# Optimization experiments

Hardware: AMD Instinct MI355X
Metric: run time of the kernel (lower is better)

## Reference

```python
import jax, jax.numpy as jnp
import numpy as np

H = 256        # hidden_size
V = 8192       # output_size / vocab
S = 4096       # encoder source length


def _lin(x, w, b):
    # torch nn.Linear: x @ W^T + b, W shape [out, in]
    return x @ w.T + b


def setup_inputs() -> dict:
    key = jax.random.key(0)
    ks = jax.random.split(key, 32)
    f32 = jnp.float32

    def w(i, shape, scale=0.02):
        return (jax.random.normal(ks[i], shape) * scale).astype(f32)

    inp = {
        "input_tok": jax.random.randint(ks[0], (1,), 0, V),
        "hidden": jax.random.normal(ks[1], (1, H), dtype=f32),
        "encoder_outputs": jax.random.normal(ks[2], (S, 2 * H), dtype=f32),
        "emb": w(3, (V, V), 0.02),
        "Uz_w": w(4, (H, V)), "Uz_b": jnp.zeros((H,), f32),
        "Wz_w": w(5, (H, H)), "Wz_b": jnp.zeros((H,), f32),
        "Cz_w": w(6, (H, 2 * H)), "Cz_b": jnp.zeros((H,), f32),
        "Ur_w": w(7, (H, V)), "Ur_b": jnp.zeros((H,), f32),
        "Wr_w": w(8, (H, H)), "Wr_b": jnp.zeros((H,), f32),
        "Cr_w": w(9, (H, 2 * H)), "Cr_b": jnp.zeros((H,), f32),
        "Uh_w": w(10, (H, V)), "Uh_b": jnp.zeros((H,), f32),
        "Wh_w": w(11, (H, H)), "Wh_b": jnp.zeros((H,), f32),
        "Ch_w": w(12, (H, 2 * H)), "Ch_b": jnp.zeros((H,), f32),
        "Ua_w": w(13, (H, 2 * H)), "Ua_b": jnp.zeros((H,), f32),
        "Wa_w": w(14, (H, H)), "Wa_b": jnp.zeros((H,), f32),
        "Va_w": w(15, (1, H)), "Va_b": jnp.zeros((1,), f32),
        "V_w": w(16, (V, H)), "V_b": jnp.zeros((V,), f32),
    }
    return inp


def reference(input_tok, hidden, encoder_outputs, emb,
              Uz_w, Uz_b, Wz_w, Wz_b, Cz_w, Cz_b,
              Ur_w, Ur_b, Wr_w, Wr_b, Cr_w, Cr_b,
              Uh_w, Uh_b, Wh_w, Wh_b, Ch_w, Ch_b,
              Ua_w, Ua_b, Wa_w, Wa_b, Va_w, Va_b,
              V_w, V_b):
    y = emb[input_tok[0]].reshape(1, V)                                   # [1, V]
    # Bahdanau additive attention over encoder states (softmax over dim 0)
    e = jnp.tanh(_lin(hidden, Wa_w, Wa_b) + _lin(encoder_outputs, Ua_w, Ua_b))  # [S, H]
    Eij = _lin(e, Va_w, Va_b)                                             # [S, 1]
    aij = jax.nn.softmax(Eij, axis=0)                                     # [S, 1]
    Ci = jnp.sum(aij * encoder_outputs, axis=0).reshape(1, 2 * H)         # [1, 2H]
    # GRU gates
    z = jax.nn.sigmoid(_lin(y, Uz_w, Uz_b) + _lin(hidden, Wz_w, Wz_b) + _lin(Ci, Cz_w, Cz_b))
    r = jax.nn.sigmoid(_lin(y, Ur_w, Ur_b) + _lin(hidden, Wr_w, Wr_b) + _lin(Ci, Cr_w, Cr_b))
    c = jnp.tanh(_lin(y, Uh_w, Uh_b) + _lin(r * hidden, Wh_w, Wh_b) + _lin(Ci, Ch_w, Ch_b))
    hidden_new = (1.0 - z) * c + z * hidden                               # [1, H]
    out = jax.nn.log_softmax(_lin(hidden_new, V_w, V_b), axis=1)          # [1, V]
    return (out, hidden_new, aij)
```

## Files before the change

kernel.cpp:

```cpp
#include <hip/hip_runtime.h>
#include <hip/hip_bf16.h>

typedef unsigned int u32;

#define HD 256
#define VD 8192
#define SD 4096
#define H2 512

#define WS_WAH   0
#define WS_STATS 320
#define WS_CI    384
#define WS_G     896
#define WS_AZR   1664
#define WS_HN    2432
#define WS_EIJ   2688

__device__ __forceinline__ float dot4(float4 a, float4 b, float acc) {
    acc = fmaf(a.x, b.x, acc); acc = fmaf(a.y, b.y, acc);
    acc = fmaf(a.z, b.z, acc); return fmaf(a.w, b.w, acc);
}
__device__ __forceinline__ float wred64(float v) {
    #pragma unroll
    for (int o = 32; o; o >>= 1) v += __shfl_xor(v, o);
    return v;
}

__global__ __launch_bounds__(256) void ka_gates(const int* __restrict__ tok,
        const float* __restrict__ emb,
        const float* __restrict__ Uz_w, const float* __restrict__ Uz_b,
        const float* __restrict__ Wz_w, const float* __restrict__ Wz_b,
        const float* __restrict__ Ur_w, const float* __restrict__ Ur_b,
        const float* __restrict__ Wr_w, const float* __restrict__ Wr_b,
        const float* __restrict__ Uh_w, const float* __restrict__ Uh_b,
        const float* __restrict__ Wa_w, const float* __restrict__ Wa_b,
        const float* __restrict__ hidden,
        float* __restrict__ G, float* __restrict__ wa_h) {
    int t = threadIdx.x, lane = t & 63, wv = t >> 6;
    if (blockIdx.x == 192) {
        __shared__ __align__(16) float hs[HD];
        hs[t] = hidden[t];
        __syncthreads();
        float acc = 0.f;
        const float4* row = (const float4*)(Wa_w + (size_t)t * HD);
        #pragma unroll 4
        for (int k = 0; k < HD / 4; ++k)
            acc = dot4(row[k], *(const float4*)&hs[k * 4], acc);
        wa_h[t] = acc + Wa_b[t];
        return;
    }
    int wg = blockIdx.x * 4 + wv;
    int g = wg >> 8, i = wg & 255;
    const float* U = (g == 0 ? Uz_w : (g == 1 ? Ur_w : Uh_w)) + (size_t)i * VD;
    const float* y = emb + (size_t)tok[0] * VD;
    float acc = 0.f;
    for (int c = 0; c < VD; c += 512) {
        int k = c + lane * 8;
        acc = dot4(*(const float4*)(U + k),     *(const float4*)(y + k),     acc);
        acc = dot4(*(const float4*)(U + k + 4), *(const float4*)(y + k + 4), acc);
    }
    if (g < 2) {
        const float* W = (g == 0 ? Wz_w : Wr_w) + (size_t)i * HD;
        int k = lane * 4;
        acc = dot4(*(const float4*)(W + k), *(const float4*)(hidden + k), acc);
    }
    acc = wred64(acc);
    if (lane == 0) {
        float b;
        if (g == 0)      b = Uz_b[i] + Wz_b[i];
        else if (g == 1) b = Ur_b[i] + Wr_b[i];
        else             b = Uh_b[i];
        G[wg] = acc + b;
    }
}

__global__ __launch_bounds__(256) void k1_scores(const float* __restrict__ enc,
        const float* __restrict__ Ua_w, const float* __restrict__ Ua_b,
        const float* __restrict__ Va_w, const float* __restrict__ Va_b,
        const float* __restrict__ wa_h, float* __restrict__ Eij) {
    __shared__ __align__(16) float encs[16 * H2];
    int t = threadIdx.x;
    int lane = t & 63, sg = t >> 6;
    int h0 = lane * 4;
    long s0 = (long)blockIdx.x * 16;

    for (int i = t * 4; i < 16 * H2; i += 1024)
        *(float4*)&encs[i] = *(const float4*)(enc + s0 * H2 + i);
    __syncthreads();

    float acc[4][4];
    #pragma unroll
    for (int a = 0; a < 4; ++a)
        #pragma unroll
        for (int b = 0; b < 4; ++b) acc[a][b] = 0.f;

    const float* r0 = Ua_w + (size_t)(h0 + 0) * H2;
    const float* r1 = Ua_w + (size_t)(h0 + 1) * H2;
    const float* r2 = Ua_w + (size_t)(h0 + 2) * H2;
    const float* r3 = Ua_w + (size_t)(h0 + 3) * H2;
    for (int kc = 0; kc < H2; kc += 4) {
        float4 a0 = *(const float4*)(r0 + kc);
        float4 a1 = *(const float4*)(r1 + kc);
        float4 a2 = *(const float4*)(r2 + kc);
        float4 a3 = *(const float4*)(r3 + kc);
        #pragma unroll
        for (int ss = 0; ss < 4; ++ss) {
            float4 ev = *(const float4*)&encs[(sg * 4 + ss) * H2 + kc];
            acc[ss][0] = dot4(a0, ev, acc[ss][0]);
            acc[ss][1] = dot4(a1, ev, acc[ss][1]);
            acc[ss][2] = dot4(a2, ev, acc[ss][2]);
            acc[ss][3] = dot4(a3, ev, acc[ss][3]);
        }
    }

    float bias[4], va[4];
    #pragma unroll
    for (int j = 0; j < 4; ++j) {
        bias[j] = wa_h[h0 + j] + Ua_b[h0 + j];
        va[j]   = Va_w[h0 + j];
    }
    float vb = Va_b[0];
    #pragma unroll
    for (int ss = 0; ss < 4; ++ss) {
        float v = 0.f;
        #pragma unroll
        for (int j = 0; j < 4; ++j)
            v += va[j] * tanhf(acc[ss][j] + bias[j]);
        v = wred64(v);
        if (lane == 0) Eij[s0 + sg * 4 + ss] = v + vb;
    }
}

__global__ __launch_bounds__(256) void k2_stats(const float* __restrict__ Eij,
                                                float* __restrict__ stats,
                                                float* __restrict__ Ci) {
    __shared__ float sh[4];
    int t = threadIdx.x, lane = t & 63, wv = t >> 6;
    float m = -1e30f;
    for (int i = t; i < SD; i += 256) m = fmaxf(m, Eij[i]);
    #pragma unroll
    for (int o = 32; o; o >>= 1) m = fmaxf(m, __shfl_xor(m, o));
    if (lane == 0) sh[wv] = m;
    __syncthreads();
    m = fmaxf(fmaxf(sh[0], sh[1]), fmaxf(sh[2], sh[3]));
    __syncthreads();
    float s = 0.f;
    for (int i = t; i < SD; i += 256) s += __expf(Eij[i] - m);
    s = wred64(s);
    if (lane == 0) sh[wv] = s;
    __syncthreads();
    s = sh[0] + sh[1] + sh[2] + sh[3];
    if (t == 0) { stats[0] = m; stats[1] = 1.f / s; }
    for (int i = t; i < H2; i += 256) Ci[i] = 0.f;
}

__global__ __launch_bounds__(256) void k3_ci(const float* __restrict__ Eij,
                                             const float* __restrict__ stats,
                                             const float* __restrict__ enc,
                                             float* __restrict__ out,
                                             float* __restrict__ Ci) {
    __shared__ float a[64];
    int t = threadIdx.x;
    long s0 = (long)blockIdx.x * 64;
    if (t < 64) {
        float v = __expf(Eij[s0 + t] - stats[0]) * stats[1];
        a[t] = v;
        out[8448 + s0 + t] = v;
    }
    __syncthreads();
    float acc0 = 0.f, acc1 = 0.f;
    for (int s = 0; s < 64; ++s) {
        float av = a[s];
        const float* r = enc + (s0 + s) * H2;
        acc0 = fmaf(av, r[t], acc0);
        acc1 = fmaf(av, r[t + 256], acc1);
    }
    atomicAdd(Ci + t, acc0);
    atomicAdd(Ci + t + 256, acc1);
}

__global__ __launch_bounds__(256) void k5a_cdots(const float* __restrict__ G,
        const float* __restrict__ Ci,
        const float* __restrict__ Cz_w, const float* __restrict__ Cz_b,
        const float* __restrict__ Cr_w, const float* __restrict__ Cr_b,
        const float* __restrict__ Ch_w, const float* __restrict__ Ch_b,
        const float* __restrict__ Wh_b,
        float* __restrict__ AZR) {
    int t = threadIdx.x, lane = t & 63, wv = t >> 6;
    int wg = blockIdx.x * 4 + wv;
    int g = wg >> 8, i = wg & 255;
    const float* C = (g == 0 ? Cz_w : (g == 1 ? Cr_w : Ch_w)) + (size_t)i * H2;
    int k = lane * 8;
    float acc = dot4(*(const float4*)(C + k),     *(const float4*)(Ci + k),     0.f);
    acc = dot4(*(const float4*)(C + k + 4), *(const float4*)(Ci + k + 4), acc);
    acc = wred64(acc);
    if (lane == 0) {
        float b;
        if (g == 0)      b = Cz_b[i];
        else if (g == 1) b = Cr_b[i];
        else             b = Wh_b[i] + Ch_b[i];
        AZR[wg] = G[wg] + acc + b;
    }
}

__global__ __launch_bounds__(256) void k5c_hnew(const float* __restrict__ AZR,
        const float* __restrict__ Wh_w, const float* __restrict__ hidden,
        float* __restrict__ hn_f, float* __restrict__ out) {
    int t = threadIdx.x, lane = t & 63, wv = t >> 6;
    int i = blockIdx.x * 4 + wv;
    int k = lane * 4;
    float4 ar4 = *(const float4*)(AZR + 256 + k);
    float4 h4  = *(const float4*)(hidden + k);
    float4 rh;
    rh.x = h4.x / (1.f + __expf(-ar4.x));
    rh.y = h4.y / (1.f + __expf(-ar4.y));
    rh.z = h4.z / (1.f + __expf(-ar4.z));
    rh.w = h4.w / (1.f + __expf(-ar4.w));
    float acc = dot4(*(const float4*)(Wh_w + (size_t)i * HD + k), rh, 0.f);
    acc = wred64(acc);
    if (lane == 0) {
        float c = tanhf(AZR[512 + i] + acc);
        float z = 1.f / (1.f + __expf(-AZR[i]));
        float hnv = (1.f - z) * c + z * hidden[i];
        hn_f[i] = hnv;
        out[8192 + i] = hnv;
    }
}

__global__ __launch_bounds__(256) void k6_logits(const float* __restrict__ Vw,
        const float* __restrict__ Vb, const float* __restrict__ hn,
        float* __restrict__ out) {
    int t = threadIdx.x, lane = t & 63, wv = t >> 6;
    float4 h4 = *(const float4*)(hn + lane * 4);
    long r0 = ((long)blockIdx.x * 4 + wv) * 16;
    for (int rr = 0; rr < 16; ++rr) {
        long j = r0 + rr;
        float acc = dot4(*(const float4*)(Vw + j * HD + lane * 4), h4, 0.f);
        acc = wred64(acc);
        if (lane == 0) out[j] = acc + Vb[j];
    }
}

__global__ __launch_bounds__(256) void k7_lsm(float* __restrict__ out) {
    __shared__ float sh[4];
    int t = threadIdx.x, lane = t & 63, wv = t >> 6;
    float m = -1e30f;
    for (int i = t; i < VD; i += 256) m = fmaxf(m, out[i]);
    #pragma unroll
    for (int o = 32; o; o >>= 1) m = fmaxf(m, __shfl_xor(m, o));
    if (lane == 0) sh[wv] = m;
    __syncthreads();
    m = fmaxf(fmaxf(sh[0], sh[1]), fmaxf(sh[2], sh[3]));
    __syncthreads();
    float s = 0.f;
    for (int i = t; i < VD; i += 256) s += __expf(out[i] - m);
    s = wred64(s);
    if (lane == 0) sh[wv] = s;
    __syncthreads();
    s = sh[0] + sh[1] + sh[2] + sh[3];
    float lse = m + __logf(s);
    for (int i = t; i < VD; i += 256) out[i] = out[i] - lse;
}

extern "C" void kernel_launch(void* const* d_in, const int* in_sizes, int n_in,
                              void* d_out, int out_size, void* d_ws, size_t ws_size,
                              hipStream_t stream) {
    const int*   tok    = (const int*)d_in[0];
    const float* hidden = (const float*)d_in[1];
    const float* enc    = (const float*)d_in[2];
    const float* emb    = (const float*)d_in[3];
    const float* Uz_w = (const float*)d_in[4],  *Uz_b = (const float*)d_in[5];
    const float* Wz_w = (const float*)d_in[6],  *Wz_b = (const float*)d_in[7];
    const float* Cz_w = (const float*)d_in[8],  *Cz_b = (const float*)d_in[9];
    const float* Ur_w = (const float*)d_in[10], *Ur_b = (const float*)d_in[11];
    const float* Wr_w = (const float*)d_in[12], *Wr_b = (const float*)d_in[13];
    const float* Cr_w = (const float*)d_in[14], *Cr_b = (const float*)d_in[15];
    const float* Uh_w = (const float*)d_in[16], *Uh_b = (const float*)d_in[17];
    const float* Wh_w = (const float*)d_in[18], *Wh_b = (const float*)d_in[19];
    const float* Ch_w = (const float*)d_in[20], *Ch_b = (const float*)d_in[21];
    const float* Ua_w = (const float*)d_in[22], *Ua_b = (const float*)d_in[23];
    const float* Wa_w = (const float*)d_in[24], *Wa_b = (const float*)d_in[25];
    const float* Va_w = (const float*)d_in[26], *Va_b = (const float*)d_in[27];
    const float* V_w  = (const float*)d_in[28], *V_b  = (const float*)d_in[29];

    float* ws    = (float*)d_ws;
    float* wa_h  = ws + WS_WAH;
    float* stats = ws + WS_STATS;
    float* Ci    = ws + WS_CI;
    float* G     = ws + WS_G;
    float* AZR   = ws + WS_AZR;
    float* hn_f  = ws + WS_HN;
    float* Eij   = ws + WS_EIJ;
    float* out   = (float*)d_out;

    ka_gates<<<193, 256, 0, stream>>>(tok, emb, Uz_w, Uz_b, Wz_w, Wz_b,
                                      Ur_w, Ur_b, Wr_w, Wr_b, Uh_w, Uh_b,
                                      Wa_w, Wa_b, hidden, G, wa_h);
    k1_scores<<<256, 256, 0, stream>>>(enc, Ua_w, Ua_b, Va_w, Va_b, wa_h, Eij);
    k2_stats<<<1, 256, 0, stream>>>(Eij, stats, Ci);
    k3_ci<<<64, 256, 0, stream>>>(Eij, stats, enc, out, Ci);
    k5a_cdots<<<192, 256, 0, stream>>>(G, Ci, Cz_w, Cz_b, Cr_w, Cr_b,
                                       Ch_w, Ch_b, Wh_b, AZR);
    k5c_hnew<<<64, 256, 0, stream>>>(AZR, Wh_w, hidden, hn_f, out);
    k6_logits<<<128, 256, 0, stream>>>(V_w, V_b, hn_f, out);
    k7_lsm<<<1, 256, 0, stream>>>(out);
}
```

Baseline: 494.7 us.

## Fuse attention and gate kernels to cut launch count from eight to five

Merges the gate GEMV and the attention score kernel into one launch. Each score block recomputes Wa·hidden redundantly, so it no longer waits on a separate producer kernel. The softmax stats are folded into the Ci kernel, with each block recomputing max and sum, and the C-dots are merged with the h_new computation, where each block recomputes the r gate. The logits kernel also emits per-block maxima so the log-softmax skips a max pass. The aim is to remove kernel launch and serialization overhead, at the cost of redundant work per block.

Result: no change. 498.4 us (+0.8%).

```diff
diff --git a/kernel.cpp b/kernel.cpp
--- a/kernel.cpp
+++ b/kernel.cpp
@@ -1,5 +1,4 @@
 #include <hip/hip_runtime.h>
-#include <hip/hip_bf16.h>
 
 typedef unsigned int u32;
 
@@ -8,11 +7,9 @@
 #define SD 4096
 #define H2 512
 
-#define WS_WAH   0
-#define WS_STATS 320
 #define WS_CI    384
 #define WS_G     896
-#define WS_AZR   1664
+#define WS_PMAX  1664
 #define WS_HN    2432
 #define WS_EIJ   2688
 
@@ -26,7 +23,7 @@
     return v;
 }
 
-__global__ __launch_bounds__(256) void ka_gates(const int* __restrict__ tok,
+__global__ __launch_bounds__(256) void ka_front(const int* __restrict__ tok,
         const float* __restrict__ emb,
         const float* __restrict__ Uz_w, const float* __restrict__ Uz_b,
         const float* __restrict__ Wz_w, const float* __restrict__ Wz_b,
@@ -34,58 +31,61 @@
         const float* __restrict__ Wr_w, const float* __restrict__ Wr_b,
         const float* __restrict__ Uh_w, const float* __restrict__ Uh_b,
         const float* __restrict__ Wa_w, const float* __restrict__ Wa_b,
-        const float* __restrict__ hidden,
-        float* __restrict__ G, float* __restrict__ wa_h) {
-    int t = threadIdx.x, lane = t & 63, wv = t >> 6;
-    if (blockIdx.x == 192) {
-        __shared__ __align__(16) float hs[HD];
-        hs[t] = hidden[t];
-        __syncthreads();
+        const float* __restrict__ Ua_w, const float* __restrict__ Ua_b,
+        const float* __restrict__ Va_w, const float* __restrict__ Va_b,
+        const float* __restrict__ enc, const float* __restrict__ hidden,
+        float* __restrict__ G, float* __restrict__ Eij, float* __restrict__ Ci) {
+    int t = threadIdx.x, lane = t & 63, wv = t >> 6;
+
+    if (blockIdx.x >= 256) {
+        int bb = blockIdx.x - 256;
+        if (bb == 0) { Ci[t] = 0.f; Ci[t + 256] = 0.f; }
+        int wg = bb * 4 + wv;
+        int g = wg >> 8, i = wg & 255;
+        const float* U = (g == 0 ? Uz_w : (g == 1 ? Ur_w : Uh_w)) + (size_t)i * VD;
+        const float* y = emb + (size_t)tok[0] * VD;
         float acc = 0.f;
-        const float4* row = (const float4*)(Wa_w + (size_t)t * HD);
+        for (int c = 0; c < VD; c += 512) {
+            int k = c + lane * 8;
+            acc = dot4(*(const float4*)(U + k),     *(const float4*)(y + k),     acc);
+            acc = dot4(*(const float4*)(U + k + 4), *(const float4*)(y + k + 4), acc);
+        }
+        if (g < 2) {
+            const float* W = (g == 0 ? Wz_w : Wr_w) + (size_t)i * HD;
+            int k = lane * 4;
+            acc = dot4(*(const float4*)(W + k), *(const float4*)(hidden + k), acc);
+        }
+        acc = wred64(acc);
+        if (lane == 0) {
+            float b;
+            if (g == 0)      b = Uz_b[i] + Wz_b[i];
+            else if (g == 1) b = Ur_b[i] + Wr_b[i];
+            else             b = Uh_b[i];
+            G[wg] = acc + b;
+        }
+        return;
+    }
+
+    __shared__ __align__(16) float encs[16 * H2];
+    __shared__ __align__(16) float hs[HD];
+    __shared__ float wah[HD];
+    int sg = wv;
+    int h0 = lane * 4;
+    long s0 = (long)blockIdx.x * 16;
+
+    for (int i = t * 4; i < 16 * H2; i += 1024)
+        *(float4*)&encs[i] = *(const float4*)(enc + s0 * H2 + i);
+    hs[t] = hidden[t];
+    __syncthreads();
+
+    {
+        float wacc = 0.f;
+        const float4* wrow = (const float4*)(Wa_w + (size_t)t * HD);
         #pragma unroll 4
         for (int k = 0; k < HD / 4; ++k)
-            acc = dot4(row[k], *(const float4*)&hs[k * 4], acc);
-        wa_h[t] = acc + Wa_b[t];
-        return;
-    }
-    int wg = blockIdx.x * 4 + wv;
-    int g = wg >> 8, i = wg & 255;
-    const float* U = (g == 0 ? Uz_w : (g == 1 ? Ur_w : Uh_w)) + (size_t)i * VD;
-    const float* y = emb + (size_t)tok[0] * VD;
-    float acc = 0.f;
-    for (int c = 0; c < VD; c += 512) {
-        int k = c + lane * 8;
-        acc = dot4(*(const float4*)(U + k),     *(const float4*)(y + k),     acc);
-        acc = dot4(*(const float4*)(U + k + 4), *(const float4*)(y + k + 4), acc);
-    }
-    if (g < 2) {
-        const float* W = (g == 0 ? Wz_w : Wr_w) + (size_t)i * HD;
-        int k = lane * 4;
-        acc = dot4(*(const float4*)(W + k), *(const float4*)(hidden + k), acc);
-    }
-    acc = wred64(acc);
-    if (lane == 0) {
-        float b;
-        if (g == 0)      b = Uz_b[i] + Wz_b[i];
-        else if (g == 1) b = Ur_b[i] + Wr_b[i];
-        else             b = Uh_b[i];
-        G[wg] = acc + b;
-    }
-}
-
-__global__ __launch_bounds__(256) void k1_scores(const float* __restrict__ enc,
-        const float* __restrict__ Ua_w, const float* __restrict__ Ua_b,
-        const float* __restrict__ Va_w, const float* __restrict__ Va_b,
-        const float* __restrict__ wa_h, float* __restrict__ Eij) {
-    __shared__ __align__(16) float encs[16 * H2];
-    int t = threadIdx.x;
-    int lane = t & 63, sg = t >> 6;
-    int h0 = lane * 4;
-    long s0 = (long)blockIdx.x * 16;
-
-    for (int i = t * 4; i < 16 * H2; i += 1024)
-        *(float4*)&encs[i] = *(const float4*)(enc + s0 * H2 + i);
+            wacc = dot4(wrow[k], *(const float4*)&hs[k * 4], wacc);
+        wah[t] = wacc + Wa_b[t] + Ua_b[t];
+    }
     __syncthreads();
 
     float acc[4][4];
@@ -116,7 +116,7 @@
     float bias[4], va[4];
     #pragma unroll
     for (int j = 0; j < 4; ++j) {
-        bias[j] = wa_h[h0 + j] + Ua_b[h0 + j];
+        bias[j] = wah[h0 + j];
         va[j]   = Va_w[h0 + j];
     }
     float vb = Va_b[0];
@@ -131,47 +131,41 @@
     }
 }
 
-__global__ __launch_bounds__(256) void k2_stats(const float* __restrict__ Eij,
-                                                float* __restrict__ stats,
-                                                float* __restrict__ Ci) {
-    __shared__ float sh[4];
-    int t = threadIdx.x, lane = t & 63, wv = t >> 6;
+__global__ __launch_bounds__(256) void kb_ci(const float* __restrict__ Eij,
+                                             const float* __restrict__ enc,
+                                             float* __restrict__ out,
+                                             float* __restrict__ Ci) {
+    __shared__ float sm[4];
+    __shared__ float a[64];
+    int t = threadIdx.x, lane = t & 63, wv = t >> 6;
+
     float m = -1e30f;
     for (int i = t; i < SD; i += 256) m = fmaxf(m, Eij[i]);
     #pragma unroll
     for (int o = 32; o; o >>= 1) m = fmaxf(m, __shfl_xor(m, o));
-    if (lane == 0) sh[wv] = m;
-    __syncthreads();
-    m = fmaxf(fmaxf(sh[0], sh[1]), fmaxf(sh[2], sh[3]));
+    if (lane == 0) sm[wv] = m;
+    __syncthreads();
+    m = fmaxf(fmaxf(sm[0], sm[1]), fmaxf(sm[2], sm[3]));
     __syncthreads();
     float s = 0.f;
     for (int i = t; i < SD; i += 256) s += __expf(Eij[i] - m);
     s = wred64(s);
-    if (lane == 0) sh[wv] = s;
-    __syncthreads();
-    s = sh[0] + sh[1] + sh[2] + sh[3];
-    if (t == 0) { stats[0] = m; stats[1] = 1.f / s; }
-    for (int i = t; i < H2; i += 256) Ci[i] = 0.f;
-}
-
-__global__ __launch_bounds__(256) void k3_ci(const float* __restrict__ Eij,
-                                             const float* __restrict__ stats,
-                                             const float* __restrict__ enc,
-                                             float* __restrict__ out,
-                                             float* __restrict__ Ci) {
-    __shared__ float a[64];
-    int t = threadIdx.x;
+    if (lane == 0) sm[wv] = s;
+    __syncthreads();
+    s = sm[0] + sm[1] + sm[2] + sm[3];
+    float rinv = 1.f / s;
+
     long s0 = (long)blockIdx.x * 64;
     if (t < 64) {
-        float v = __expf(Eij[s0 + t] - stats[0]) * stats[1];
+        float v = __expf(Eij[s0 + t] - m) * rinv;
         a[t] = v;
         out[8448 + s0 + t] = v;
     }
     __syncthreads();
     float acc0 = 0.f, acc1 = 0.f;
-    for (int s = 0; s < 64; ++s) {
-        float av = a[s];
-        const float* r = enc + (s0 + s) * H2;
+    for (int ss = 0; ss < 64; ++ss) {
+        float av = a[ss];
+        const float* r = enc + (s0 + ss) * H2;
         acc0 = fmaf(av, r[t], acc0);
         acc1 = fmaf(av, r[t + 256], acc1);
     }
@@ -179,48 +173,47 @@
     atomicAdd(Ci + t + 256, acc1);
 }
 
-__global__ __launch_bounds__(256) void k5a_cdots(const float* __restrict__ G,
+__global__ __launch_bounds__(256) void kc_hnew(const float* __restrict__ G,
         const float* __restrict__ Ci,
         const float* __restrict__ Cz_w, const float* __restrict__ Cz_b,
         const float* __restrict__ Cr_w, const float* __restrict__ Cr_b,
         const float* __restrict__ Ch_w, const float* __restrict__ Ch_b,
-        const float* __restrict__ Wh_b,
-        float* __restrict__ AZR) {
-    int t = threadIdx.x, lane = t & 63, wv = t >> 6;
-    int wg = blockIdx.x * 4 + wv;
-    int g = wg >> 8, i = wg & 255;
-    const float* C = (g == 0 ? Cz_w : (g == 1 ? Cr_w : Ch_w)) + (size_t)i * H2;
-    int k = lane * 8;
-    float acc = dot4(*(const float4*)(C + k),     *(const float4*)(Ci + k),     0.f);
-    acc = dot4(*(const float4*)(C + k + 4), *(const float4*)(Ci + k + 4), acc);
-    acc = wred64(acc);
+        const float* __restrict__ Wh_w, const float* __restrict__ Wh_b,
+        const float* __restrict__ hidden,
+        float* __restrict__ hn_f, float* __restrict__ out) {
+    __shared__ __align__(16) float cis[H2];
+    __shared__ __align__(16) float rh[HD];
+    int t = threadIdx.x, lane = t & 63, wv = t >> 6;
+
+    if (t < 128) *(float4*)&cis[t * 4] = *(const float4*)(Ci + t * 4);
+    __syncthreads();
+
+    {
+        float acc = 0.f;
+        const float4* cr = (const float4*)(Cr_w + (size_t)t * H2);
+        #pragma unroll 4
+        for (int k = 0; k < H2 / 4; ++k)
+            acc = dot4(cr[k], *(const float4*)&cis[k * 4], acc);
+        float arv = G[256 + t] + acc + Cr_b[t];
+        rh[t] = hidden[t] / (1.f + __expf(-arv));
+    }
+    __syncthreads();
+
+    int i = blockIdx.x * 4 + wv;
+    int k8 = lane * 8;
+    const float* Cz = Cz_w + (size_t)i * H2;
+    const float* Ch = Ch_w + (size_t)i * H2;
+    float az = dot4(*(const float4*)(Cz + k8),     *(const float4*)&cis[k8],     0.f);
+    az       = dot4(*(const float4*)(Cz + k8 + 4), *(const float4*)&cis[k8 + 4], az);
+    float ah = dot4(*(const float4*)(Ch + k8),     *(const float4*)&cis[k8],     0.f);
+    ah       = dot4(*(const float4*)(Ch + k8 + 4), *(const float4*)&cis[k8 + 4], ah);
+    float aw = dot4(*(const float4*)(Wh_w + (size_t)i * HD + lane * 4),
+                    *(const float4*)&rh[lane * 4], 0.f);
+    az = wred64(az); ah = wred64(ah); aw = wred64(aw);
     if (lane == 0) {
-        float b;
-        if (g == 0)      b = Cz_b[i];
-        else if (g == 1) b = Cr_b[i];
-        else             b = Wh_b[i] + Ch_b[i];
-        AZR[wg] = G[wg] + acc + b;
-    }
-}
-
-__global__ __launch_bounds__(256) void k5c_hnew(const float* __restrict__ AZR,
-        const float* __restrict__ Wh_w, const float* __restrict__ hidden,
-        float* __restrict__ hn_f, float* __restrict__ out) {
-    int t = threadIdx.x, lane = t & 63, wv = t >> 6;
-    int i = blockIdx.x * 4 + wv;
-    int k = lane * 4;
-    float4 ar4 = *(const float4*)(AZR + 256 + k);
-    float4 h4  = *(const float4*)(hidden + k);
-    float4 rh;
-    rh.x = h4.x / (1.f + __expf(-ar4.x));
-    rh.y = h4.y / (1.f + __expf(-ar4.y));
-    rh.z = h4.z / (1.f + __expf(-ar4.z));
-    rh.w = h4.w / (1.f + __expf(-ar4.w));
-    float acc = dot4(*(const float4*)(Wh_w + (size_t)i * HD + k), rh, 0.f);
-    acc = wred64(acc);
-    if (lane == 0) {
-        float c = tanhf(AZR[512 + i] + acc);
-        float z = 1.f / (1.f + __expf(-AZR[i]));
+        float z  = 1.f / (1.f + __expf(-(G[i] + az + Cz_b[i])));
+        float pc = G[512 + i] + ah + Ch_b[i] + Wh_b[i];
+        float c  = tanhf(pc + aw);
         float hnv = (1.f - z) * c + z * hidden[i];
         hn_f[i] = hnv;
         out[8192 + i] = hnv;
@@ -229,23 +222,30 @@
 
 __global__ __launch_bounds__(256) void k6_logits(const float* __restrict__ Vw,
         const float* __restrict__ Vb, const float* __restrict__ hn,
-        float* __restrict__ out) {
+        float* __restrict__ out, float* __restrict__ pmax) {
+    __shared__ float bm[4];
     int t = threadIdx.x, lane = t & 63, wv = t >> 6;
     float4 h4 = *(const float4*)(hn + lane * 4);
     long r0 = ((long)blockIdx.x * 4 + wv) * 16;
+    float pm = -1e30f;
     for (int rr = 0; rr < 16; ++rr) {
         long j = r0 + rr;
         float acc = dot4(*(const float4*)(Vw + j * HD + lane * 4), h4, 0.f);
         acc = wred64(acc);
-        if (lane == 0) out[j] = acc + Vb[j];
-    }
-}
-
-__global__ __launch_bounds__(256) void k7_lsm(float* __restrict__ out) {
+        float lg = acc + Vb[j];
+        if (lane == 0) out[j] = lg;
+        pm = fmaxf(pm, lg);
+    }
+    if (lane == 0) bm[wv] = pm;
+    __syncthreads();
+    if (t == 0) pmax[blockIdx.x] = fmaxf(fmaxf(bm[0], bm[1]), fmaxf(bm[2], bm[3]));
+}
+
+__global__ __launch_bounds__(256) void k7_lsm(float* __restrict__ out,
+                                              const float* __restrict__ pmax) {
     __shared__ float sh[4];
     int t = threadIdx.x, lane = t & 63, wv = t >> 6;
-    float m = -1e30f;
-    for (int i = t; i < VD; i += 256) m = fmaxf(m, out[i]);
+    float m = (t < 128) ? pmax[t] : -1e30f;
     #pragma unroll
     for (int o = 32; o; o >>= 1) m = fmaxf(m, __shfl_xor(m, o));
     if (lane == 0) sh[wv] = m;
@@ -284,24 +284,20 @@
     const float* V_w  = (const float*)d_in[28], *V_b  = (const float*)d_in[29];
 
     float* ws    = (float*)d_ws;
-    float* wa_h  = ws + WS_WAH;
-    float* stats = ws + WS_STATS;
     float* Ci    = ws + WS_CI;
     float* G     = ws + WS_G;
-    float* AZR   = ws + WS_AZR;
+    float* pmax  = ws + WS_PMAX;
     float* hn_f  = ws + WS_HN;
     float* Eij   = ws + WS_EIJ;
     float* out   = (float*)d_out;
 
-    ka_gates<<<193, 256, 0, stream>>>(tok, emb, Uz_w, Uz_b, Wz_w, Wz_b,
+    ka_front<<<448, 256, 0, stream>>>(tok, emb, Uz_w, Uz_b, Wz_w, Wz_b,
                                       Ur_w, Ur_b, Wr_w, Wr_b, Uh_w, Uh_b,
-                                      Wa_w, Wa_b, hidden, G, wa_h);
-    k1_scores<<<256, 256, 0, stream>>>(enc, Ua_w, Ua_b, Va_w, Va_b, wa_h, Eij);
-    k2_stats<<<1, 256, 0, stream>>>(Eij, stats, Ci);
-    k3_ci<<<64, 256, 0, stream>>>(Eij, stats, enc, out, Ci);
-    k5a_cdots<<<192, 256, 0, stream>>>(G, Ci, Cz_w, Cz_b, Cr_w, Cr_b,
-                                       Ch_w, Ch_b, Wh_b, AZR);
-    k5c_hnew<<<64, 256, 0, stream>>>(AZR, Wh_w, hidden, hn_f, out);
-    k6_logits<<<128, 256, 0, stream>>>(V_w, V_b, hn_f, out);
-    k7_lsm<<<1, 256, 0, stream>>>(out);
-}
+                                      Wa_w, Wa_b, Ua_w, Ua_b, Va_w, Va_b,
+                                      enc, hidden, G, Eij, Ci);
+    kb_ci<<<64, 256, 0, stream>>>(Eij, enc, out, Ci);
+    kc_hnew<<<64, 256, 0, stream>>>(G, Ci, Cz_w, Cz_b, Cr_w, Cr_b,
+                                    Ch_w, Ch_b, Wh_w, Wh_b, hidden, hn_f, out);
+    k6_logits<<<128, 256, 0, stream>>>(V_w, V_b, hn_f, out, pmax);
+    k7_lsm<<<1, 256, 0, stream>>>(out, pmax);
+}
```
